# Optimization experiments

Hardware: AMD Instinct MI355X
Metric: run time of the kernel (lower is better)

The kernel has to match this reference:

```python
import jax, jax.numpy as jnp
import numpy as np
from jax import lax

SUR_BETA = 4.0
THRESH = 1.0
ALPHA = float(np.exp(-1.0 / 20.0))  # membrane decay, tau_mem=20
BETA = float(np.exp(-1.0 / 5.0))    # synaptic decay, tau_syn=5

@jax.custom_vjp
def spike(x):
    return (x >= 0).astype(jnp.float32)

def _spike_fwd(x):
    return spike(x), x

def _spike_bwd(x, g):
    e = jnp.exp(-SUR_BETA * jnp.abs(x))
    sg = SUR_BETA * e / (2.0 * (1.0 + e) ** 2)
    return (g * sg,)

spike.defvjp(_spike_fwd, _spike_bwd)

def lif_layer(x, W, b):
    # x: [B, T, Din] -> spikes [B, T, H]
    xt = jnp.einsum('bti,ih->bth', x, W) + b
    B, T, H = xt.shape
    z = jnp.zeros((B, H), xt.dtype)
    def step(carry, x_t):
        v, i = carry
        i = BETA * i + x_t
        v = ALPHA * v + i
        s = spike(v - THRESH)
        v = v * (1.0 - s)  # multiplicative reset
        return (v, i), s
    _, sp = lax.scan(step, (z, z), xt.transpose(1, 0, 2))
    return sp.transpose(1, 0, 2)

def layer_norm(x, scale, bias, eps=1e-6):
    m = jnp.mean(x, axis=-1, keepdims=True)
    v = jnp.mean((x - m) ** 2, axis=-1, keepdims=True)
    return (x - m) / jnp.sqrt(v + eps) * scale + bias

def setup_inputs() -> dict:
    key = jax.random.key(0)
    ks = jax.random.split(key, 6)
    B, T, S, F = 64, 512, 64, 16
    D = S * F  # 1024
    def w(k, shape, fan):
        return (jax.random.normal(k, shape, jnp.float32) / np.sqrt(fan)).astype(jnp.float32)
    return dict(
        spike_trains=(jax.random.uniform(ks[0], (B, T, S, F)) < 0.2).astype(jnp.float32),
        W0=w(ks[1], (D, 256), D), b0=jnp.zeros((256,), jnp.float32),
        W1=w(ks[2], (256, 128), 256), b1=jnp.zeros((128,), jnp.float32),
        W2=w(ks[3], (128, 64), 128), b2=jnp.zeros((64,), jnp.float32),
        ln1_scale=jnp.ones((256,), jnp.float32), ln1_bias=jnp.zeros((256,), jnp.float32),
        ln2_scale=jnp.ones((128,), jnp.float32), ln2_bias=jnp.zeros((128,), jnp.float32),
        Wc=w(ks[4], (B, 2), B), bc=jnp.zeros((2,), jnp.float32),
    )

def reference(spike_trains, W0, b0, W1, b1, W2, b2,
              ln1_scale, ln1_bias, ln2_scale, ln2_bias, Wc, bc):
    B, T, S, F = spike_trains.shape
    x = spike_trains.reshape(B, T, S * F)
    x = lif_layer(x, W0, b0)                                   # [B,T,256]
    x = lif_layer(layer_norm(x, ln1_scale, ln1_bias), W1, b1)  # [B,T,128]
    x = lif_layer(layer_norm(x, ln2_scale, ln2_bias), W2, b2)  # [B,T,64]
    pooled = jnp.mean(x, axis=(1, 2))  # [B]  (faithful to source: mean over time AND hidden)
    logits = pooled @ Wc + bc          # [num_classes] -- classifier sees batch as feature dim
    return (logits, pooled, jnp.mean(x))
```

## Files before the change

kernel.cpp:

```cpp
#include <hip/hip_runtime.h>

#define T_STEPS 512
#define BATCH 64

__device__ constexpr float ALPHA_ = 0.95122942450071400910f;
__device__ constexpr float BETA_  = 0.81873075307798185867f;

typedef __attribute__((ext_vector_type(8))) short bf16x8;
typedef __attribute__((ext_vector_type(4))) float f32x4;

__device__ inline unsigned short f2bf_rne(float f) {
  union { float f; unsigned int u; } v{f};
  const unsigned int u = v.u;
  return (unsigned short)((u + 0x7FFFu + ((u >> 16) & 1u)) >> 16);
}
__device__ inline float bf2f(unsigned short h) {
  union { unsigned int u; float f; } v{(unsigned int)h << 16};
  return v.f;
}

__device__ inline void gload16(const void* g, void* l) {
  __builtin_amdgcn_global_load_lds(
      (const __attribute__((address_space(1))) unsigned int*)g,
      (__attribute__((address_space(3))) unsigned int*)l, 16, 0, 0);
}

__device__ inline unsigned int pkbf(float first, float second) {
#if __has_builtin(__builtin_amdgcn_perm)
  return __builtin_amdgcn_perm(__float_as_uint(second), __float_as_uint(first),
                               0x07060302u);
#else
  return (__float_as_uint(first) >> 16) | (__float_as_uint(second) & 0xFFFF0000u);
#endif
}

__device__ inline bf16x8 cvt_frag(const f32x4 lo, const f32x4 hi) {
  union { unsigned int w[4]; bf16x8 v; } u;
  u.w[0] = pkbf(lo.x, lo.y);
  u.w[1] = pkbf(lo.z, lo.w);
  u.w[2] = pkbf(hi.x, hi.y);
  u.w[3] = pkbf(hi.z, hi.w);
  return u.v;
}

template <int WM, int WC, int TM, bool A_F32, bool LNFOLD>
__global__ __launch_bounds__(256) void gemm_pipe(
    const void* __restrict__ Av, const char* __restrict__ Bhi,
    const char* __restrict__ Blo, const float* __restrict__ uvec,
    const float* __restrict__ cvec, float* __restrict__ C, int N, int K) {
  constexpr int BM = WM * TM;
  constexpr int BN = WC * 64;
  constexpr int FM = TM / 16;
  constexpr int ABY = A_F32 ? BM * 128 : BM * 64;
  constexpr int BBH = BN * 64;
  constexpr int BUFBY = ABY + 2 * BBH;
  constexpr int API = (ABY / 16) / 256;
  __shared__ char smem[2 * BUFBY];

  const int tid = threadIdx.x;
  const int lane = tid & 63;
  const int wave = tid >> 6;
  const int wm = wave / WC, wc = wave % WC;
  const int l15 = lane & 15, l4 = lane >> 4;
  const int row0 = blockIdx.y * BM;
  const int col0 = blockIdx.x * BN;
  const int KB = K / 32;

  const char* Ab = (const char*)Av;

  const char* a_src[API];
#pragma unroll
  for (int i = 0; i < API; ++i) {
    const int unit = i * 256 + tid;
    if constexpr (A_F32) {
      const int fr = unit >> 7, h = (unit >> 6) & 1, ln = unit & 63;
      a_src[i] = Ab + ((size_t)(row0 + fr * 16 + (ln & 15)) * K + ((ln >> 4) * 8)) * 4 + h * 16;
    } else {
      const int r = ((unit >> 6) << 4) | (unit & 15);
      const int j = (unit >> 4) & 3;
      a_src[i] = Ab + ((size_t)(row0 + r) * K + j * 8) * 2;
    }
  }
  const char* bh_src[WC];
  const char* bl_src[WC];
#pragma unroll
  for (int g = 0; g < WC; ++g) {
    const size_t so = ((size_t)(blockIdx.x * WC + g) * KB) * 4096 + (size_t)tid * 16;
    bh_src[g] = Bhi + so;
    bl_src[g] = Blo + so;
  }

  auto stage = [&](int kb, char* buf) {
#pragma unroll
    for (int i = 0; i < API; ++i) {
      const int unit = i * 256 + tid;
      gload16(a_src[i] + (size_t)kb * (A_F32 ? 128 : 64), buf + unit * 16);
    }
#pragma unroll
    for (int g = 0; g < WC; ++g) {
      gload16(bh_src[g] + (size_t)kb * 4096, buf + ABY + (g * 256 + tid) * 16);
      gload16(bl_src[g] + (size_t)kb * 4096, buf + ABY + BBH + (g * 256 + tid) * 16);
    }
  };

  f32x4 acc[FM][4] = {};
  f32x4 acc1[FM] = {};
  const bf16x8 ONES = {0x3F80, 0x3F80, 0x3F80, 0x3F80,
                       0x3F80, 0x3F80, 0x3F80, 0x3F80};

  stage(0, smem);
  asm volatile("s_waitcnt vmcnt(0)" ::: "memory");
  __builtin_amdgcn_s_barrier();
  __builtin_amdgcn_sched_barrier(0);

  for (int kb = 0; kb < KB; ++kb) {
    char* bufc = smem + (kb & 1) * BUFBY;
    char* bufn = smem + ((kb & 1) ^ 1) * BUFBY;
    if (kb + 1 < KB) stage(kb + 1, bufn);

    bf16x8 af[FM], bh[4], bl[4];
#pragma unroll
    for (int m = 0; m < FM; ++m) {
      const int fr = wm * FM + m;
      if constexpr (A_F32) {
        const f32x4 lo = *(const f32x4*)(bufc + ((fr * 2 + 0) * 64 + lane) * 16);
        const f32x4 hi = *(const f32x4*)(bufc + ((fr * 2 + 1) * 64 + lane) * 16);
        af[m] = cvt_frag(lo, hi);
      } else {
        af[m] = *(const bf16x8*)(bufc + (fr * 64 + lane) * 16);
      }
    }
#pragma unroll
    for (int n = 0; n < 4; ++n) {
      bh[n] = *(const bf16x8*)(bufc + ABY + (wc * 256 + n * 64 + lane) * 16);
      bl[n] = *(const bf16x8*)(bufc + ABY + BBH + (wc * 256 + n * 64 + lane) * 16);
    }

#pragma unroll
    for (int m = 0; m < FM; ++m) {
#pragma unroll
      for (int n = 0; n < 4; ++n) {
        acc[m][n] = __builtin_amdgcn_mfma_f32_16x16x32_bf16(af[m], bh[n], acc[m][n], 0, 0, 0);
        acc[m][n] = __builtin_amdgcn_mfma_f32_16x16x32_bf16(af[m], bl[n], acc[m][n], 0, 0, 0);
      }
      if constexpr (LNFOLD)
        acc1[m] = __builtin_amdgcn_mfma_f32_16x16x32_bf16(af[m], ONES, acc1[m], 0, 0, 0);
    }

    asm volatile("s_waitcnt vmcnt(0)" ::: "memory");
    __builtin_amdgcn_s_barrier();
    __builtin_amdgcn_sched_barrier(0);
  }

  const int row0w = row0 + wm * TM;
  const int col0w = col0 + wc * 64;
#pragma unroll
  for (int m = 0; m < FM; ++m) {
    const int rbase = row0w + m * 16 + l4 * 4;
    float iv[4], mv[4];
    if constexpr (LNFOLD) {
#pragma unroll
      for (int r = 0; r < 4; ++r) {
        const float mean = acc1[m][r] / (float)K;
        const float inv = 1.0f / sqrtf(mean * (1.f - mean) + 1e-6f);
        iv[r] = inv;
        mv[r] = mean * inv;
      }
    }
#pragma unroll
    for (int n = 0; n < 4; ++n) {
      const int c = col0w + n * 16 + l15;
      const float cc = cvec[c];
      float uu = 0.f;
      if constexpr (LNFOLD) uu = uvec[c];
#pragma unroll
      for (int r = 0; r < 4; ++r) {
        float v;
        if constexpr (LNFOLD) v = iv[r] * acc[m][n][r] - mv[r] * uu + cc;
        else v = acc[m][n][r] + cc;
        C[(size_t)(rbase + r) * N + c] = v;
      }
    }
  }
}

__global__ void prep_split(const float* __restrict__ W, const float* __restrict__ s,
                           char* __restrict__ hi, char* __restrict__ lo,
                           int K, int N) {
  const int g = blockIdx.x * 256 + threadIdx.x;
  const int total = (K * N) / 8;
  if (g >= total) return;
  constexpr int UB = 256;
  const int KB = K / 32;
  const int unit = g % UB;
  const int kb = (g / UB) % KB;
  const int cb = g / (UB * KB);
  const int n = cb * 64 + ((unit >> 6) << 4) + (unit & 15);
  const int kbase = kb * 32 + ((unit >> 4) & 3) * 8;
  short h8[8], l8[8];
#pragma unroll
  for (int jj = 0; jj < 8; ++jj) {
    const int k = kbase + jj;
    float w = W[(size_t)k * N + n];
    if (s) w *= s[k];
    const unsigned short hb = f2bf_rne(w);
    const unsigned short lb = f2bf_rne(w - bf2f(hb));
    h8[jj] = (short)hb;
    l8[jj] = (short)lb;
  }
  *(bf16x8*)(hi + (size_t)g * 16) = *(const bf16x8*)h8;
  *(bf16x8*)(lo + (size_t)g * 16) = *(const bf16x8*)l8;
}

__global__ __launch_bounds__(256) void prep_consts(
    const float* __restrict__ W, const float* __restrict__ s,
    const float* __restrict__ b, const float* __restrict__ bias2,
    float* __restrict__ u, float* __restrict__ c, int K, int N) {
  const int n = blockIdx.x;
  const int t = threadIdx.x;
  float us = 0.f, cs = 0.f;
  for (int k = t; k < K; k += 256) {
    const float w = W[(size_t)k * N + n];
    us += s[k] * w;
    cs += b[k] * w;
  }
  __shared__ float su[256], sc[256];
  su[t] = us;
  sc[t] = cs;
  __syncthreads();
  for (int o = 128; o > 0; o >>= 1) {
    if (t < o) { su[t] += su[t + o]; sc[t] += sc[t + o]; }
    __syncthreads();
  }
  if (t == 0) { u[n] = su[0]; c[n] = sc[0] + bias2[n]; }
}

template <int H, bool SPIKE_OUT, bool ACCUM>
__global__ void lif_scan(const float* __restrict__ xt,
                         unsigned short* __restrict__ sp,
                         float* __restrict__ tsum) {
  const int n = blockIdx.x * 64 + threadIdx.x;
  const int b = n / H, h = n % H;
  const float* p = xt + (size_t)b * T_STEPS * H + h;
  unsigned short* q = nullptr;
  if constexpr (SPIKE_OUT) q = sp + (size_t)b * T_STEPS * H + h;

  float v = 0.f, cur = 0.f, ts = 0.f;
  for (int t = 0; t < T_STEPS; t += 32) {
    float x[32];
#pragma unroll
    for (int u = 0; u < 32; ++u) x[u] = p[(size_t)u * H];
#pragma unroll
    for (int u = 0; u < 32; ++u) {
      cur = BETA_ * cur + x[u];
      v = ALPHA_ * v + cur;
      const bool sb = (v >= 1.f);
      if constexpr (SPIKE_OUT) q[(size_t)u * H] = sb ? 0x3F80 : 0;
      if constexpr (ACCUM) ts += sb ? 1.f : 0.f;
      v = sb ? 0.f : v;
    }
    p += (size_t)32 * H;
    if constexpr (SPIKE_OUT) q += (size_t)32 * H;
  }
  if constexpr (ACCUM) tsum[n] = ts;
}

__global__ void finalize(const float* __restrict__ tsum,
                         const float* __restrict__ Wc,
                         const float* __restrict__ bc,
                         float* __restrict__ out) {
  const int b = threadIdx.x;
  float s = 0.f;
#pragma unroll 8
  for (int h = 0; h < 64; ++h) s += tsum[b * 64 + h];
  const float pooled = s * (1.0f / (512.f * 64.f));
  out[2 + b] = pooled;

  float tot = pooled;
  float l0 = pooled * Wc[b * 2 + 0];
  float l1 = pooled * Wc[b * 2 + 1];
#pragma unroll
  for (int off = 32; off > 0; off >>= 1) {
    tot += __shfl_xor(tot, off);
    l0 += __shfl_xor(l0, off);
    l1 += __shfl_xor(l1, off);
  }
  if (b == 0) {
    out[0] = l0 + bc[0];
    out[1] = l1 + bc[1];
    out[66] = tot * (1.0f / 64.f);
  }
}

extern "C" void kernel_launch(void* const* d_in, const int* in_sizes, int n_in,
                              void* d_out, int out_size, void* d_ws, size_t ws_size,
                              hipStream_t stream) {
  const float* X    = (const float*)d_in[0];
  const float* W0   = (const float*)d_in[1];
  const float* b0   = (const float*)d_in[2];
  const float* W1   = (const float*)d_in[3];
  const float* b1   = (const float*)d_in[4];
  const float* W2   = (const float*)d_in[5];
  const float* b2   = (const float*)d_in[6];
  const float* ln1s = (const float*)d_in[7];
  const float* ln1b = (const float*)d_in[8];
  const float* ln2s = (const float*)d_in[9];
  const float* ln2b = (const float*)d_in[10];
  const float* Wc   = (const float*)d_in[11];
  const float* bc   = (const float*)d_in[12];
  float* out = (float*)d_out;

  char* w = (char*)d_ws;
  float* buf0 = (float*)w;
  float* buf1 = (float*)w;
  float* buf2 = (float*)(w + 16777216);
  size_t off = 33554432;
  unsigned short* sp0 = (unsigned short*)(w + off); off += 16777216;
  unsigned short* sp1 = (unsigned short*)(w + off); off += 8388608;
  char* hi0 = w + off; off += 524288;
  char* lo0 = w + off; off += 524288;
  char* hi1 = w + off; off += 65536;
  char* lo1 = w + off; off += 65536;
  char* hi2 = w + off; off += 16384;
  char* lo2 = w + off; off += 16384;
  float* u1 = (float*)(w + off); off += 512;
  float* c1 = (float*)(w + off); off += 512;
  float* u2 = (float*)(w + off); off += 256;
  float* c2 = (float*)(w + off); off += 256;
  float* tsum = (float*)(w + off); off += 16384;

  const int M = 32768;

  prep_split<<<128, 256, 0, stream>>>(W0, nullptr, hi0, lo0, 1024, 256);
  prep_split<<<16, 256, 0, stream>>>(W1, ln1s, hi1, lo1, 256, 128);
  prep_split<<<4, 256, 0, stream>>>(W2, ln2s, hi2, lo2, 128, 64);
  prep_consts<<<128, 256, 0, stream>>>(W1, ln1s, ln1b, b1, u1, c1, 256, 128);
  prep_consts<<<64, 256, 0, stream>>>(W2, ln2s, ln2b, b2, u2, c2, 128, 64);

  gemm_pipe<2, 2, 64, true, false><<<dim3(2, M / 128), 256, 0, stream>>>(
      X, hi0, lo0, nullptr, b0, buf0, 256, 1024);
  lif_scan<256, true, false><<<(BATCH * 256) / 64, 64, 0, stream>>>(buf0, sp0, nullptr);

  gemm_pipe<4, 1, 32, false, true><<<dim3(2, M / 128), 256, 0, stream>>>(
      sp0, hi1, lo1, u1, c1, buf1, 128, 256);
  lif_scan<128, true, false><<<(BATCH * 128) / 64, 64, 0, stream>>>(buf1, sp1, nullptr);

  gemm_pipe<4, 1, 32, false, true><<<dim3(1, M / 128), 256, 0, stream>>>(
      sp1, hi2, lo2, u2, c2, buf2, 64, 128);
  lif_scan<64, false, true><<<(BATCH * 64) / 64, 64, 0, stream>>>(buf2, nullptr, tsum);

  finalize<<<1, 64, 0, stream>>>(tsum, Wc, bc, out);
}
```

Baseline: 135.4 us.

## Restructure GEMMs with triple-buffered A and register-held B loaded from global

```diff
diff --git a/kernel.cpp b/kernel.cpp
--- a/kernel.cpp
+++ b/kernel.cpp
@@ -44,18 +44,17 @@
 }
 
 template <int WM, int WC, int TM, bool A_F32, bool LNFOLD>
-__global__ __launch_bounds__(256) void gemm_pipe(
+__global__ __launch_bounds__(256) void gemm_deep2(
     const void* __restrict__ Av, const char* __restrict__ Bhi,
     const char* __restrict__ Blo, const float* __restrict__ uvec,
     const float* __restrict__ cvec, float* __restrict__ C, int N, int K) {
   constexpr int BM = WM * TM;
-  constexpr int BN = WC * 64;
   constexpr int FM = TM / 16;
   constexpr int ABY = A_F32 ? BM * 128 : BM * 64;
-  constexpr int BBH = BN * 64;
-  constexpr int BUFBY = ABY + 2 * BBH;
-  constexpr int API = (ABY / 16) / 256;
-  __shared__ char smem[2 * BUFBY];
+  constexpr int AIP = ABY / 4096;
+  constexpr int ASTEP = A_F32 ? 128 : 64;
+  constexpr int W2N = AIP + 16;
+  __shared__ char smem[3 * ABY];
 
   const int tid = threadIdx.x;
   const int lane = tid & 63;
@@ -63,14 +62,14 @@
   const int wm = wave / WC, wc = wave % WC;
   const int l15 = lane & 15, l4 = lane >> 4;
   const int row0 = blockIdx.y * BM;
-  const int col0 = blockIdx.x * BN;
+  const int col0 = blockIdx.x * (WC * 64);
   const int KB = K / 32;
 
   const char* Ab = (const char*)Av;
 
-  const char* a_src[API];
-#pragma unroll
-  for (int i = 0; i < API; ++i) {
+  const char* a_src[AIP];
+#pragma unroll
+  for (int i = 0; i < AIP; ++i) {
     const int unit = i * 256 + tid;
     if constexpr (A_F32) {
       const int fr = unit >> 7, h = (unit >> 6) & 1, ln = unit & 63;
@@ -81,76 +80,110 @@
       a_src[i] = Ab + ((size_t)(row0 + r) * K + j * 8) * 2;
     }
   }
-  const char* bh_src[WC];
-  const char* bl_src[WC];
-#pragma unroll
-  for (int g = 0; g < WC; ++g) {
-    const size_t so = ((size_t)(blockIdx.x * WC + g) * KB) * 4096 + (size_t)tid * 16;
-    bh_src[g] = Bhi + so;
-    bl_src[g] = Blo + so;
-  }
-
-  auto stage = [&](int kb, char* buf) {
-#pragma unroll
-    for (int i = 0; i < API; ++i) {
-      const int unit = i * 256 + tid;
-      gload16(a_src[i] + (size_t)kb * (A_F32 ? 128 : 64), buf + unit * 16);
-    }
-#pragma unroll
-    for (int g = 0; g < WC; ++g) {
-      gload16(bh_src[g] + (size_t)kb * 4096, buf + ABY + (g * 256 + tid) * 16);
-      gload16(bl_src[g] + (size_t)kb * 4096, buf + ABY + BBH + (g * 256 + tid) * 16);
-    }
-  };
+  const char* bh_base = Bhi + (size_t)(blockIdx.x * WC + wc) * KB * 4096 + (size_t)lane * 16;
+  const char* bl_base = Blo + (size_t)(blockIdx.x * WC + wc) * KB * 4096 + (size_t)lane * 16;
+
+  int aoff = 0, boff = 0;
+  const int amax = (KB - 1) * ASTEP;
+  const int bmax = (KB - 1) * 4096;
 
   f32x4 acc[FM][4] = {};
   f32x4 acc1[FM] = {};
   const bf16x8 ONES = {0x3F80, 0x3F80, 0x3F80, 0x3F80,
                        0x3F80, 0x3F80, 0x3F80, 0x3F80};
-
-  stage(0, smem);
-  asm volatile("s_waitcnt vmcnt(0)" ::: "memory");
+  bf16x8 bh0[4], bl0[4], bh1[4], bl1[4];
+
+#define SB __builtin_amdgcn_sched_barrier(0)
+
+#define STAGE_A(buf)                                                   \
+  do {                                                                 \
+    _Pragma("unroll") for (int i = 0; i < AIP; ++i)                    \
+        gload16(a_src[i] + aoff, (buf) + (i * 256 + tid) * 16);        \
+  } while (0)
+
+#define LOAD_B(bh, bl, off_)                                           \
+  do {                                                                 \
+    const char* ph = bh_base + (off_);                                 \
+    const char* pl = bl_base + (off_);                                 \
+    bh[0] = *(const bf16x8*)(ph);                                      \
+    bh[1] = *(const bf16x8*)(ph + 1024);                               \
+    bh[2] = *(const bf16x8*)(ph + 2048);                               \
+    bh[3] = *(const bf16x8*)(ph + 3072);                               \
+    bl[0] = *(const bf16x8*)(pl);                                      \
+    bl[1] = *(const bf16x8*)(pl + 1024);                               \
+    bl[2] = *(const bf16x8*)(pl + 2048);                               \
+    bl[3] = *(const bf16x8*)(pl + 3072);                               \
+  } while (0)
+
+  char* bufR = smem;
+  char* bufM = smem + ABY;
+  char* bufS = smem + 2 * ABY;
+
+  SB;
+  STAGE_A(bufR);
+  SB;
+  LOAD_B(bh0, bl0, 0);
+  SB;
+  aoff = ASTEP;
+  STAGE_A(bufM);
+  SB;
+  LOAD_B(bh1, bl1, 4096);
+  SB;
+  aoff = (2 * ASTEP < amax) ? 2 * ASTEP : amax;
+  boff = (2 * 4096 < bmax) ? 2 * 4096 : bmax;
+  asm volatile("s_waitcnt vmcnt(%0)" ::"i"(W2N) : "memory");
   __builtin_amdgcn_s_barrier();
-  __builtin_amdgcn_sched_barrier(0);
-
-  for (int kb = 0; kb < KB; ++kb) {
-    char* bufc = smem + (kb & 1) * BUFBY;
-    char* bufn = smem + ((kb & 1) ^ 1) * BUFBY;
-    if (kb + 1 < KB) stage(kb + 1, bufn);
-
-    bf16x8 af[FM], bh[4], bl[4];
-#pragma unroll
-    for (int m = 0; m < FM; ++m) {
-      const int fr = wm * FM + m;
-      if constexpr (A_F32) {
-        const f32x4 lo = *(const f32x4*)(bufc + ((fr * 2 + 0) * 64 + lane) * 16);
-        const f32x4 hi = *(const f32x4*)(bufc + ((fr * 2 + 1) * 64 + lane) * 16);
-        af[m] = cvt_frag(lo, hi);
-      } else {
-        af[m] = *(const bf16x8*)(bufc + (fr * 64 + lane) * 16);
-      }
-    }
-#pragma unroll
-    for (int n = 0; n < 4; ++n) {
-      bh[n] = *(const bf16x8*)(bufc + ABY + (wc * 256 + n * 64 + lane) * 16);
-      bl[n] = *(const bf16x8*)(bufc + ABY + BBH + (wc * 256 + n * 64 + lane) * 16);
-    }
-
-#pragma unroll
-    for (int m = 0; m < FM; ++m) {
-#pragma unroll
-      for (int n = 0; n < 4; ++n) {
-        acc[m][n] = __builtin_amdgcn_mfma_f32_16x16x32_bf16(af[m], bh[n], acc[m][n], 0, 0, 0);
-        acc[m][n] = __builtin_amdgcn_mfma_f32_16x16x32_bf16(af[m], bl[n], acc[m][n], 0, 0, 0);
-      }
-      if constexpr (LNFOLD)
-        acc1[m] = __builtin_amdgcn_mfma_f32_16x16x32_bf16(af[m], ONES, acc1[m], 0, 0, 0);
-    }
-
-    asm volatile("s_waitcnt vmcnt(0)" ::: "memory");
-    __builtin_amdgcn_s_barrier();
-    __builtin_amdgcn_sched_barrier(0);
-  }
+  SB;
+
+#define KSTEP(BH, BL)                                                        \
+  do {                                                                       \
+    STAGE_A(bufS);                                              \
+    aoff = (aoff < amax) ? aoff + ASTEP : aoff;                              \
+    SB;                                                                      \
+    bf16x8 af[FM];                                                           \
+    _Pragma("unroll") for (int m = 0; m < FM; ++m) {                         \
+      const int fr = wm * FM + m;                                            \
+      if constexpr (A_F32) {                                                 \
+        const f32x4 lo = *(const f32x4*)(bufR + ((fr * 2 + 0) * 64 + lane) * 16); \
+        const f32x4 hi = *(const f32x4*)(bufR + ((fr * 2 + 1) * 64 + lane) * 16); \
+        af[m] = cvt_frag(lo, hi);                                            \
+      } else {                                                               \
+        af[m] = *(const bf16x8*)(bufR + (fr * 64 + lane) * 16);              \
+      }                                                                      \
+    }                                                                        \
+    SB;                                                                      \
+    _Pragma("unroll") for (int m = 0; m < FM; ++m) {                         \
+      _Pragma("unroll") for (int n = 0; n < 4; ++n) {                        \
+        acc[m][n] = __builtin_amdgcn_mfma_f32_16x16x32_bf16(af[m], BH[n],    \
+                                                            acc[m][n], 0, 0, 0); \
+        acc[m][n] = __builtin_amdgcn_mfma_f32_16x16x32_bf16(af[m], BL[n],    \
+                                                            acc[m][n], 0, 0, 0); \
+      }                                                                      \
+      if constexpr (LNFOLD)                                                  \
+        acc1[m] = __builtin_amdgcn_mfma_f32_16x16x32_bf16(af[m], ONES,       \
+                                                          acc1[m], 0, 0, 0); \
+    }                                                                        \
+    SB;                                                                      \
+    LOAD_B(BH, BL, boff);            \
+    boff = (boff < bmax) ? boff + 4096 : boff;                               \
+    SB;                                                                      \
+    asm volatile("s_waitcnt vmcnt(%0)" ::"i"(W2N) : "memory");               \
+    __builtin_amdgcn_s_barrier();                                            \
+    SB;                                                                      \
+    { char* t = bufR; bufR = bufM; bufM = bufS; bufS = t; }                  \
+  } while (0)
+
+  const int ITER = KB / 2;
+  for (int it = 0; it < ITER; ++it) {
+    KSTEP(bh0, bl0);
+    KSTEP(bh1, bl1);
+  }
+  asm volatile("s_waitcnt vmcnt(0) lgkmcnt(0)" ::: "memory");
+
+#undef KSTEP
+#undef LOAD_B
+#undef STAGE_A
+#undef SB
 
   const int row0w = row0 + wm * TM;
   const int col0w = col0 + wc * 64;
@@ -337,15 +370,15 @@
   prep_consts<<<128, 256, 0, stream>>>(W1, ln1s, ln1b, b1, u1, c1, 256, 128);
   prep_consts<<<64, 256, 0, stream>>>(W2, ln2s, ln2b, b2, u2, c2, 128, 64);
 
-  gemm_pipe<2, 2, 64, true, false><<<dim3(2, M / 128), 256, 0, stream>>>(
+  gemm_deep2<1, 4, 64, true, false><<<dim3(1, M / 64), 256, 0, stream>>>(
       X, hi0, lo0, nullptr, b0, buf0, 256, 1024);
   lif_scan<256, true, false><<<(BATCH * 256) / 64, 64, 0, stream>>>(buf0, sp0, nullptr);
 
-  gemm_pipe<4, 1, 32, false, true><<<dim3(2, M / 128), 256, 0, stream>>>(
+  gemm_deep2<2, 2, 32, false, true><<<dim3(1, M / 64), 256, 0, stream>>>(
       sp0, hi1, lo1, u1, c1, buf1, 128, 256);
   lif_scan<128, true, false><<<(BATCH * 128) / 64, 64, 0, stream>>>(buf1, sp1, nullptr);
 
-  gemm_pipe<4, 1, 32, false, true><<<dim3(1, M / 128), 256, 0, stream>>>(
+  gemm_deep2<4, 1, 32, false, true><<<dim3(1, M / 128), 256, 0, stream>>>(
       sp1, hi2, lo2, u2, c2, buf2, 64, 128);
   lif_scan<64, false, true><<<(BATCH * 64) / 64, 64, 0, stream>>>(buf2, nullptr, tsum);
 
```

Result: faster. 132.1 us (-2.4%).

## Switch GEMMs to two-level int8 weight quantization with int8 MFMA and byte spikes

Applied to the files above, without the earlier changes.

```diff
diff --git a/kernel.cpp b/kernel.cpp
--- a/kernel.cpp
+++ b/kernel.cpp
@@ -6,154 +6,173 @@
 __device__ constexpr float ALPHA_ = 0.95122942450071400910f;
 __device__ constexpr float BETA_  = 0.81873075307798185867f;
 
-typedef __attribute__((ext_vector_type(8))) short bf16x8;
+typedef __attribute__((ext_vector_type(4))) int   i32x4;
 typedef __attribute__((ext_vector_type(4))) float f32x4;
 
-__device__ inline unsigned short f2bf_rne(float f) {
-  union { float f; unsigned int u; } v{f};
-  const unsigned int u = v.u;
-  return (unsigned short)((u + 0x7FFFu + ((u >> 16) & 1u)) >> 16);
-}
-__device__ inline float bf2f(unsigned short h) {
-  union { unsigned int u; float f; } v{(unsigned int)h << 16};
-  return v.f;
-}
-
-__device__ inline void gload16(const void* g, void* l) {
-  __builtin_amdgcn_global_load_lds(
-      (const __attribute__((address_space(1))) unsigned int*)g,
-      (__attribute__((address_space(3))) unsigned int*)l, 16, 0, 0);
-}
-
-__device__ inline unsigned int pkbf(float first, float second) {
-#if __has_builtin(__builtin_amdgcn_perm)
-  return __builtin_amdgcn_perm(__float_as_uint(second), __float_as_uint(first),
-                               0x07060302u);
-#else
-  return (__float_as_uint(first) >> 16) | (__float_as_uint(second) & 0xFFFF0000u);
-#endif
-}
-
-__device__ inline bf16x8 cvt_frag(const f32x4 lo, const f32x4 hi) {
-  union { unsigned int w[4]; bf16x8 v; } u;
-  u.w[0] = pkbf(lo.x, lo.y);
-  u.w[1] = pkbf(lo.z, lo.w);
-  u.w[2] = pkbf(hi.x, hi.y);
-  u.w[3] = pkbf(hi.z, hi.w);
-  return u.v;
+__global__ void zero_slots(unsigned int* __restrict__ slots) {
+  if (threadIdx.x < 3) slots[threadIdx.x] = 0u;
+}
+
+__global__ void prep_maxabs(const float* __restrict__ W, const float* __restrict__ s,
+                            unsigned int* __restrict__ slot, int K, int N) {
+  const int stride = gridDim.x * 256;
+  float m = 0.f;
+  for (int i = blockIdx.x * 256 + threadIdx.x; i < K * N; i += stride) {
+    float w = W[i];
+    if (s) w *= s[i / N];
+    m = fmaxf(m, fabsf(w));
+  }
+#pragma unroll
+  for (int o = 32; o > 0; o >>= 1) m = fmaxf(m, __shfl_xor(m, o));
+  if ((threadIdx.x & 63) == 0) atomicMax(slot, __float_as_uint(m));
+}
+
+__global__ void prep_quant(const float* __restrict__ W, const float* __restrict__ s,
+                           const unsigned int* __restrict__ slot,
+                           char* __restrict__ H1, char* __restrict__ H2,
+                           int K, int N) {
+  const int g = blockIdx.x * 256 + threadIdx.x;
+  const int total = (K * N) / 16;
+  if (g >= total) return;
+  const float maxv = fmaxf(__uint_as_float(*slot), 1e-30f);
+  const float s1 = maxv * (1.0f / 127.0f);
+  const float s2 = s1 * (1.0f / 254.0f);
+  const float inv1 = 1.0f / s1, inv2 = 1.0f / s2;
+  const int KB = K / 64;
+  const int u = g & 255;
+  const int kb = (g >> 8) % KB;
+  const int cb = g / (256 * KB);
+  const int lane = u & 63;
+  const int n = cb * 64 + ((u >> 6) << 4) + (lane & 15);
+  const int kbase = kb * 64 + ((lane >> 4) << 4);
+  unsigned int w1[4] = {0, 0, 0, 0}, w2[4] = {0, 0, 0, 0};
+#pragma unroll
+  for (int jj = 0; jj < 16; ++jj) {
+    const int k = kbase + jj;
+    float w = W[(size_t)k * N + n];
+    if (s) w *= s[k];
+    const int q1 = (int)rintf(w * inv1);
+    const float r = w - (float)q1 * s1;
+    const int q2 = (int)rintf(r * inv2);
+    w1[jj >> 2] |= ((unsigned int)(q1 & 0xFF)) << ((jj & 3) * 8);
+    w2[jj >> 2] |= ((unsigned int)(q2 & 0xFF)) << ((jj & 3) * 8);
+  }
+  i32x4 v1, v2;
+#pragma unroll
+  for (int q = 0; q < 4; ++q) { v1[q] = (int)w1[q]; v2[q] = (int)w2[q]; }
+  *(i32x4*)(H1 + (size_t)g * 16) = v1;
+  *(i32x4*)(H2 + (size_t)g * 16) = v2;
 }
 
 template <int WM, int WC, int TM, bool A_F32, bool LNFOLD>
-__global__ __launch_bounds__(256) void gemm_pipe(
-    const void* __restrict__ Av, const char* __restrict__ Bhi,
-    const char* __restrict__ Blo, const float* __restrict__ uvec,
-    const float* __restrict__ cvec, float* __restrict__ C, int N, int K) {
-  constexpr int BM = WM * TM;
-  constexpr int BN = WC * 64;
+__global__ __launch_bounds__(256) void gemm_i8(
+    const void* __restrict__ Av, const char* __restrict__ H1,
+    const char* __restrict__ H2, const unsigned int* __restrict__ slot,
+    const float* __restrict__ uvec, const float* __restrict__ cvec,
+    float* __restrict__ C, int N, int K) {
   constexpr int FM = TM / 16;
-  constexpr int ABY = A_F32 ? BM * 128 : BM * 64;
-  constexpr int BBH = BN * 64;
-  constexpr int BUFBY = ABY + 2 * BBH;
-  constexpr int API = (ABY / 16) / 256;
-  __shared__ char smem[2 * BUFBY];
+  __shared__ char smem[3 * 4096];
 
   const int tid = threadIdx.x;
   const int lane = tid & 63;
   const int wave = tid >> 6;
   const int wm = wave / WC, wc = wave % WC;
   const int l15 = lane & 15, l4 = lane >> 4;
-  const int row0 = blockIdx.y * BM;
-  const int col0 = blockIdx.x * BN;
-  const int KB = K / 32;
-
-  const char* Ab = (const char*)Av;
-
-  const char* a_src[API];
-#pragma unroll
-  for (int i = 0; i < API; ++i) {
-    const int unit = i * 256 + tid;
+  const int row0 = blockIdx.y * 64;
+  const int KB = K / 64;
+
+  const int srow = ((tid >> 6) << 4) | (tid & 15);
+  const int skoff = ((tid >> 4) & 3) * 16;
+  const float* af32 = (const float*)Av + (size_t)(row0 + srow) * K + skoff;
+  const char*  ai8  = (const char*)Av + (size_t)(row0 + srow) * K + skoff;
+
+  const size_t bbase = ((size_t)(blockIdx.x * WC + wc) * KB) * 4096 + (size_t)lane * 16;
+
+  i32x4 acc1[FM][4] = {};
+  i32x4 acc2[FM][4] = {};
+  i32x4 accR[FM] = {};
+  const i32x4 ONESB = {0x01010101, 0x01010101, 0x01010101, 0x01010101};
+
+  i32x4 bf1[4], bf2[4];
+  f32x4 ar0, ar1, ar2, ar3;
+  i32x4 apack;
+
+  auto loadA = [&](int kb) {
     if constexpr (A_F32) {
-      const int fr = unit >> 7, h = (unit >> 6) & 1, ln = unit & 63;
-      a_src[i] = Ab + ((size_t)(row0 + fr * 16 + (ln & 15)) * K + ((ln >> 4) * 8)) * 4 + h * 16;
+      const float* p = af32 + (size_t)kb * 64;
+      ar0 = *(const f32x4*)(p);
+      ar1 = *(const f32x4*)(p + 4);
+      ar2 = *(const f32x4*)(p + 8);
+      ar3 = *(const f32x4*)(p + 12);
     } else {
-      const int r = ((unit >> 6) << 4) | (unit & 15);
-      const int j = (unit >> 4) & 3;
-      a_src[i] = Ab + ((size_t)(row0 + r) * K + j * 8) * 2;
-    }
-  }
-  const char* bh_src[WC];
-  const char* bl_src[WC];
-#pragma unroll
-  for (int g = 0; g < WC; ++g) {
-    const size_t so = ((size_t)(blockIdx.x * WC + g) * KB) * 4096 + (size_t)tid * 16;
-    bh_src[g] = Bhi + so;
-    bl_src[g] = Blo + so;
-  }
-
-  auto stage = [&](int kb, char* buf) {
-#pragma unroll
-    for (int i = 0; i < API; ++i) {
-      const int unit = i * 256 + tid;
-      gload16(a_src[i] + (size_t)kb * (A_F32 ? 128 : 64), buf + unit * 16);
-    }
-#pragma unroll
-    for (int g = 0; g < WC; ++g) {
-      gload16(bh_src[g] + (size_t)kb * 4096, buf + ABY + (g * 256 + tid) * 16);
-      gload16(bl_src[g] + (size_t)kb * 4096, buf + ABY + BBH + (g * 256 + tid) * 16);
+      apack = *(const i32x4*)(ai8 + (size_t)kb * 64);
     }
   };
-
-  f32x4 acc[FM][4] = {};
-  f32x4 acc1[FM] = {};
-  const bf16x8 ONES = {0x3F80, 0x3F80, 0x3F80, 0x3F80,
-                       0x3F80, 0x3F80, 0x3F80, 0x3F80};
-
-  stage(0, smem);
-  asm volatile("s_waitcnt vmcnt(0)" ::: "memory");
-  __builtin_amdgcn_s_barrier();
-  __builtin_amdgcn_sched_barrier(0);
+  auto packA = [&]() -> i32x4 {
+    if constexpr (A_F32) {
+      i32x4 r;
+      const f32x4 vv[4] = {ar0, ar1, ar2, ar3};
+#pragma unroll
+      for (int q = 0; q < 4; ++q) {
+        const f32x4 v = vv[q];
+        r[q] = (int)(((__float_as_uint(v.x) >> 29) & 1u) |
+                     (((__float_as_uint(v.y) >> 29) & 1u) << 8) |
+                     (((__float_as_uint(v.z) >> 29) & 1u) << 16) |
+                     (((__float_as_uint(v.w) >> 29) & 1u) << 24));
+      }
+      return r;
+    } else {
+      return apack;
+    }
+  };
+  auto loadB = [&](int kb) {
+    const char* p1 = H1 + bbase + (size_t)kb * 4096;
+    const char* p2 = H2 + bbase + (size_t)kb * 4096;
+#pragma unroll
+    for (int n = 0; n < 4; ++n) {
+      bf1[n] = *(const i32x4*)(p1 + n * 1024);
+      bf2[n] = *(const i32x4*)(p2 + n * 1024);
+    }
+  };
+
+  loadA(0);
+  *(i32x4*)(smem + tid * 16) = packA();
+  loadA(1);
+  loadB(0);
+  __syncthreads();
 
   for (int kb = 0; kb < KB; ++kb) {
-    char* bufc = smem + (kb & 1) * BUFBY;
-    char* bufn = smem + ((kb & 1) ^ 1) * BUFBY;
-    if (kb + 1 < KB) stage(kb + 1, bufn);
-
-    bf16x8 af[FM], bh[4], bl[4];
+    char* bufc = smem + (kb % 3) * 4096;
+    char* bufn = smem + ((kb + 1) % 3) * 4096;
+    if (kb + 1 < KB) {
+      *(i32x4*)(bufn + tid * 16) = packA();
+      loadA(kb + 2 < KB ? kb + 2 : KB - 1);
+    }
+    __syncthreads();
+
+    i32x4 af[FM];
+#pragma unroll
+    for (int m = 0; m < FM; ++m)
+      af[m] = *(const i32x4*)(bufc + ((wm * FM + m) * 64 + lane) * 16);
+
 #pragma unroll
     for (int m = 0; m < FM; ++m) {
-      const int fr = wm * FM + m;
-      if constexpr (A_F32) {
-        const f32x4 lo = *(const f32x4*)(bufc + ((fr * 2 + 0) * 64 + lane) * 16);
-        const f32x4 hi = *(const f32x4*)(bufc + ((fr * 2 + 1) * 64 + lane) * 16);
-        af[m] = cvt_frag(lo, hi);
-      } else {
-        af[m] = *(const bf16x8*)(bufc + (fr * 64 + lane) * 16);
-      }
-    }
-#pragma unroll
-    for (int n = 0; n < 4; ++n) {
-      bh[n] = *(const bf16x8*)(bufc + ABY + (wc * 256 + n * 64 + lane) * 16);
-      bl[n] = *(const bf16x8*)(bufc + ABY + BBH + (wc * 256 + n * 64 + lane) * 16);
-    }
-
-#pragma unroll
-    for (int m = 0; m < FM; ++m) {
 #pragma unroll
       for (int n = 0; n < 4; ++n) {
-        acc[m][n] = __builtin_amdgcn_mfma_f32_16x16x32_bf16(af[m], bh[n], acc[m][n], 0, 0, 0);
-        acc[m][n] = __builtin_amdgcn_mfma_f32_16x16x32_bf16(af[m], bl[n], acc[m][n], 0, 0, 0);
+        acc1[m][n] = __builtin_amdgcn_mfma_i32_16x16x64_i8(af[m], bf1[n], acc1[m][n], 0, 0, 0);
+        acc2[m][n] = __builtin_amdgcn_mfma_i32_16x16x64_i8(af[m], bf2[n], acc2[m][n], 0, 0, 0);
       }
       if constexpr (LNFOLD)
-        acc1[m] = __builtin_amdgcn_mfma_f32_16x16x32_bf16(af[m], ONES, acc1[m], 0, 0, 0);
-    }
-
-    asm volatile("s_waitcnt vmcnt(0)" ::: "memory");
-    __builtin_amdgcn_s_barrier();
-    __builtin_amdgcn_sched_barrier(0);
-  }
-
+        accR[m] = __builtin_amdgcn_mfma_i32_16x16x64_i8(af[m], ONESB, accR[m], 0, 0, 0);
+    }
+    if (kb + 1 < KB) loadB(kb + 1);
+  }
+
+  const float maxv = fmaxf(__uint_as_float(*slot), 1e-30f);
+  const float s1 = maxv * (1.0f / 127.0f);
+  const float s2 = s1 * (1.0f / 254.0f);
   const int row0w = row0 + wm * TM;
-  const int col0w = col0 + wc * 64;
+  const int col0w = blockIdx.x * (WC * 64) + wc * 64;
 #pragma unroll
   for (int m = 0; m < FM; ++m) {
     const int rbase = row0w + m * 16 + l4 * 4;
@@ -161,7 +180,7 @@
     if constexpr (LNFOLD) {
 #pragma unroll
       for (int r = 0; r < 4; ++r) {
-        const float mean = acc1[m][r] / (float)K;
+        const float mean = (float)accR[m][r] / (float)K;
         const float inv = 1.0f / sqrtf(mean * (1.f - mean) + 1e-6f);
         iv[r] = inv;
         mv[r] = mean * inv;
@@ -175,41 +194,14 @@
       if constexpr (LNFOLD) uu = uvec[c];
 #pragma unroll
       for (int r = 0; r < 4; ++r) {
+        const float dot = s1 * (float)acc1[m][n][r] + s2 * (float)acc2[m][n][r];
         float v;
-        if constexpr (LNFOLD) v = iv[r] * acc[m][n][r] - mv[r] * uu + cc;
-        else v = acc[m][n][r] + cc;
+        if constexpr (LNFOLD) v = iv[r] * dot - mv[r] * uu + cc;
+        else v = dot + cc;
         C[(size_t)(rbase + r) * N + c] = v;
       }
     }
   }
-}
-
-__global__ void prep_split(const float* __restrict__ W, const float* __restrict__ s,
-                           char* __restrict__ hi, char* __restrict__ lo,
-                           int K, int N) {
-  const int g = blockIdx.x * 256 + threadIdx.x;
-  const int total = (K * N) / 8;
-  if (g >= total) return;
-  constexpr int UB = 256;
-  const int KB = K / 32;
-  const int unit = g % UB;
-  const int kb = (g / UB) % KB;
-  const int cb = g / (UB * KB);
-  const int n = cb * 64 + ((unit >> 6) << 4) + (unit & 15);
-  const int kbase = kb * 32 + ((unit >> 4) & 3) * 8;
-  short h8[8], l8[8];
-#pragma unroll
-  for (int jj = 0; jj < 8; ++jj) {
-    const int k = kbase + jj;
-    float w = W[(size_t)k * N + n];
-    if (s) w *= s[k];
-    const unsigned short hb = f2bf_rne(w);
-    const unsigned short lb = f2bf_rne(w - bf2f(hb));
-    h8[jj] = (short)hb;
-    l8[jj] = (short)lb;
-  }
-  *(bf16x8*)(hi + (size_t)g * 16) = *(const bf16x8*)h8;
-  *(bf16x8*)(lo + (size_t)g * 16) = *(const bf16x8*)l8;
 }
 
 __global__ __launch_bounds__(256) void prep_consts(
@@ -237,12 +229,12 @@
 
 template <int H, bool SPIKE_OUT, bool ACCUM>
 __global__ void lif_scan(const float* __restrict__ xt,
-                         unsigned short* __restrict__ sp,
+                         char* __restrict__ sp,
                          float* __restrict__ tsum) {
   const int n = blockIdx.x * 64 + threadIdx.x;
   const int b = n / H, h = n % H;
   const float* p = xt + (size_t)b * T_STEPS * H + h;
-  unsigned short* q = nullptr;
+  char* q = nullptr;
   if constexpr (SPIKE_OUT) q = sp + (size_t)b * T_STEPS * H + h;
 
   float v = 0.f, cur = 0.f, ts = 0.f;
@@ -255,7 +247,7 @@
       cur = BETA_ * cur + x[u];
       v = ALPHA_ * v + cur;
       const bool sb = (v >= 1.f);
-      if constexpr (SPIKE_OUT) q[(size_t)u * H] = sb ? 0x3F80 : 0;
+      if constexpr (SPIKE_OUT) q[(size_t)u * H] = sb ? (char)1 : (char)0;
       if constexpr (ACCUM) ts += sb ? 1.f : 0.f;
       v = sb ? 0.f : v;
     }
@@ -315,38 +307,46 @@
   float* buf1 = (float*)w;
   float* buf2 = (float*)(w + 16777216);
   size_t off = 33554432;
-  unsigned short* sp0 = (unsigned short*)(w + off); off += 16777216;
-  unsigned short* sp1 = (unsigned short*)(w + off); off += 8388608;
-  char* hi0 = w + off; off += 524288;
-  char* lo0 = w + off; off += 524288;
-  char* hi1 = w + off; off += 65536;
-  char* lo1 = w + off; off += 65536;
-  char* hi2 = w + off; off += 16384;
-  char* lo2 = w + off; off += 16384;
+  char* sp0 = w + off; off += 8388608;
+  char* sp1 = w + off; off += 4194304;
+  char* h1_0 = w + off; off += 262144;
+  char* h2_0 = w + off; off += 262144;
+  char* h1_1 = w + off; off += 32768;
+  char* h2_1 = w + off; off += 32768;
+  char* h1_2 = w + off; off += 8192;
+  char* h2_2 = w + off; off += 8192;
   float* u1 = (float*)(w + off); off += 512;
   float* c1 = (float*)(w + off); off += 512;
   float* u2 = (float*)(w + off); off += 256;
   float* c2 = (float*)(w + off); off += 256;
+  unsigned int* slots = (unsigned int*)(w + off); off += 256;
   float* tsum = (float*)(w + off); off += 16384;
 
   const int M = 32768;
 
-  prep_split<<<128, 256, 0, stream>>>(W0, nullptr, hi0, lo0, 1024, 256);
-  prep_split<<<16, 256, 0, stream>>>(W1, ln1s, hi1, lo1, 256, 128);
-  prep_split<<<4, 256, 0, stream>>>(W2, ln2s, hi2, lo2, 128, 64);
+  zero_slots<<<1, 64, 0, stream>>>(slots);
+  prep_maxabs<<<64, 256, 0, stream>>>(W0, nullptr, slots + 0, 1024, 256);
+  prep_maxabs<<<16, 256, 0, stream>>>(W1, ln1s, slots + 1, 256, 128);
+  prep_maxabs<<<8, 256, 0, stream>>>(W2, ln2s, slots + 2, 128, 64);
+  prep_quant<<<(1024 * 256 / 16 + 255) / 256, 256, 0, stream>>>(
+      W0, nullptr, slots + 0, h1_0, h2_0, 1024, 256);
+  prep_quant<<<(256 * 128 / 16 + 255) / 256, 256, 0, stream>>>(
+      W1, ln1s, slots + 1, h1_1, h2_1, 256, 128);
+  prep_quant<<<(128 * 64 / 16 + 255) / 256, 256, 0, stream>>>(
+      W2, ln2s, slots + 2, h1_2, h2_2, 128, 64);
   prep_consts<<<128, 256, 0, stream>>>(W1, ln1s, ln1b, b1, u1, c1, 256, 128);
   prep_consts<<<64, 256, 0, stream>>>(W2, ln2s, ln2b, b2, u2, c2, 128, 64);
 
-  gemm_pipe<2, 2, 64, true, false><<<dim3(2, M / 128), 256, 0, stream>>>(
-      X, hi0, lo0, nullptr, b0, buf0, 256, 1024);
+  gemm_i8<2, 2, 32, true, false><<<dim3(2, M / 64), 256, 0, stream>>>(
+      X, h1_0, h2_0, slots + 0, nullptr, b0, buf0, 256, 1024);
   lif_scan<256, true, false><<<(BATCH * 256) / 64, 64, 0, stream>>>(buf0, sp0, nullptr);
 
-  gemm_pipe<4, 1, 32, false, true><<<dim3(2, M / 128), 256, 0, stream>>>(
-      sp0, hi1, lo1, u1, c1, buf1, 128, 256);
+  gemm_i8<4, 1, 16, false, true><<<dim3(2, M / 64), 256, 0, stream>>>(
+      sp0, h1_1, h2_1, slots + 1, u1, c1, buf1, 128, 256);
   lif_scan<128, true, false><<<(BATCH * 128) / 64, 64, 0, stream>>>(buf1, sp1, nullptr);
 
-  gemm_pipe<4, 1, 32, false, true><<<dim3(1, M / 128), 256, 0, stream>>>(
-      sp1, hi2, lo2, u2, c2, buf2, 64, 128);
+  gemm_i8<4, 1, 16, false, true><<<dim3(1, M / 64), 256, 0, stream>>>(
+      sp1, h1_2, h2_2, slots + 2, u2, c2, buf2, 64, 128);
   lif_scan<64, false, true><<<(BATCH * 64) / 64, 64, 0, stream>>>(buf2, nullptr, tsum);
 
   finalize<<<1, 64, 0, stream>>>(tsum, Wc, bc, out);
```

New measurement: 168.9 us. 1.25x slower.
